# Performance work log

Measured on AMD Instinct MI355X. Metric: run time of the kernel, lower is better.

## Reference

```python
import jax, jax.numpy as jnp
import numpy as np


def setup_inputs() -> dict:
    key = jax.random.key(0)
    k1, k2 = jax.random.split(key)
    inputs = jax.random.normal(k1, (32, 4096, 64), dtype=jnp.float32)
    embed = jax.random.normal(k2, (64, 1024), dtype=jnp.float32)  # [embed_dim, n_embed]
    return {"inputs": inputs, "embed": embed}


def reference(inputs, embed):
    # Eval-mode forward of VectorQuantizer (self.training == False, no EMA update).
    embed_dim, n_embed = embed.shape
    flat = inputs.reshape(-1, embed_dim)  # [N, D]
    # distances[n, k] = ||flat_n||^2 - 2 flat_n . e_k + ||e_k||^2
    distances = (
        jnp.sum(flat * flat, axis=1, keepdims=True)
        - 2.0 * (flat @ embed)
        + jnp.sum(embed * embed, axis=0, keepdims=True)
    )  # [N, n_embed]
    # torch.argmax(-distances, 1) == argmin(distances, 1) (same first-occurrence tie-break)
    encoding_indices = jnp.argmin(distances, axis=1)  # [N] int
    idx = encoding_indices.reshape(inputs.shape[:-1])  # [B, T]
    # quantize: F.embedding(idx, embed.T) -> gather rows of embed.T
    quantized = jnp.take(embed.T, idx, axis=0)  # [B, T, D]
    codes = jnp.concatenate([inputs, quantized], axis=-1)  # [B, T, 2D]
    # straight-through estimator
    quantized_st = inputs + jax.lax.stop_gradient(quantized - inputs)
    return quantized_st, codes, idx
```

## Files before the change

### kernel.cpp

```cpp
#include <hip/hip_runtime.h>

#define D 64
#define KCODES 1024
#define PTS_PER_BLK 256
#define MTILES 16
#define NT 4
#define CODE_CHUNKS 4
#define PTILES 512
#define WL_CAP 4096

typedef short bf16x8 __attribute__((ext_vector_type(8)));
typedef float f32x4 __attribute__((ext_vector_type(4)));

static __device__ __forceinline__ short f2bf(float f) {
  unsigned u = __float_as_uint(f);
  u += 0x7FFF + ((u >> 16) & 1);
  return (short)(u >> 16);
}

static __device__ __forceinline__ void evalExact(const float* __restrict__ inputs,
                                                 const float* __restrict__ embedT,
                                                 const float* __restrict__ en2,
                                                 const float* s_fn2,
                                                 int p0blk, int pl, int c,
                                                 unsigned long long* s_best) {
  int p = p0blk + pl;
  const float* f = inputs + (size_t)p * D;
  const float* e = embedT + (size_t)c * D;
  float a0 = 0.f, a1 = 0.f, a2 = 0.f, a3 = 0.f;
#pragma unroll
  for (int d = 0; d < D; d += 4) {
    a0 = fmaf(f[d + 0], e[d + 0], a0);
    a1 = fmaf(f[d + 1], e[d + 1], a1);
    a2 = fmaf(f[d + 2], e[d + 2], a2);
    a3 = fmaf(f[d + 3], e[d + 3], a3);
  }
  float dot = (a0 + a1) + (a2 + a3);
  float dist = fmaf(-2.f, dot, s_fn2[pl]) + en2[c];
  unsigned long long key = ((unsigned long long)__float_as_uint(dist) << 32) | (unsigned)c;
  atomicMin(&s_best[pl], key);
}

__global__ void __launch_bounds__(256) vq_prep(const float* __restrict__ embed,
                                               const float* __restrict__ inputs,
                                               float* __restrict__ embedT,
                                               unsigned short* __restrict__ embedTb,
                                               float* __restrict__ en2,
                                               int* __restrict__ en2max_bits,
                                               float* __restrict__ fn2,
                                               unsigned long long* __restrict__ best) {
  const int bid = blockIdx.x;
  const int tid = threadIdx.x;
  if (bid < KCODES / 256) {
    int k = bid * 256 + tid;
    float row[D];
    float s = 0.f;
#pragma unroll
    for (int d = 0; d < D; ++d) {
      float e = embed[d * KCODES + k];
      row[d] = e;
      s = fmaf(e, e, s);
    }
    en2[k] = s;
    float4* o4 = reinterpret_cast<float4*>(embedT + (size_t)k * D);
#pragma unroll
    for (int j = 0; j < 16; ++j)
      o4[j] = make_float4(row[4 * j], row[4 * j + 1], row[4 * j + 2], row[4 * j + 3]);
    unsigned us[32];
#pragma unroll
    for (int j = 0; j < 32; ++j) {
      unsigned lo = (unsigned short)f2bf(row[2 * j]);
      unsigned hi = (unsigned short)f2bf(row[2 * j + 1]);
      us[j] = lo | (hi << 16);
    }
    uint4* ob = reinterpret_cast<uint4*>(embedTb + (size_t)k * D);
#pragma unroll
    for (int j = 0; j < 8; ++j)
      ob[j] = make_uint4(us[4 * j], us[4 * j + 1], us[4 * j + 2], us[4 * j + 3]);
    float m = s;
#pragma unroll
    for (int off = 32; off; off >>= 1) m = fmaxf(m, __shfl_down(m, off, 64));
    if ((tid & 63) == 0) atomicMax(en2max_bits, __float_as_int(m));
  } else {
    int p = (bid - KCODES / 256) * 256 + tid;
    const float4* i4 = reinterpret_cast<const float4*>(inputs + (size_t)p * D);
    float s = 0.f;
#pragma unroll
    for (int j = 0; j < 16; ++j) {
      float4 v = i4[j];
      s = fmaf(v.x, v.x, s); s = fmaf(v.y, v.y, s);
      s = fmaf(v.z, v.z, s); s = fmaf(v.w, v.w, s);
    }
    fn2[p] = s;
    best[p] = ~0ull;
  }
}

__global__ void __launch_bounds__(256, 4) vq_partial(
    const float* __restrict__ inputs, const float* __restrict__ embedT,
    const unsigned short* __restrict__ embedTb, const float* __restrict__ en2,
    const float* __restrict__ fn2, const int* __restrict__ en2max_bits,
    unsigned long long* __restrict__ best) {
  __shared__ unsigned long long s_best[PTS_PER_BLK];
  __shared__ unsigned s_wl[WL_CAP];
  __shared__ int s_wcount;
  __shared__ float s_fn2[PTS_PER_BLK];
  __shared__ float s_wmin[4][16];

  const int tid = threadIdx.x;
  const int w = tid >> 6;
  const int l = tid & 63;
  const int l15 = l & 15;
  const int lg = l >> 4;
  const int chunk = blockIdx.x / PTILES;
  const int ptile = blockIdx.x % PTILES;
  const int p0blk = ptile * PTS_PER_BLK;
  const int cb = chunk * 256 + w * 64;

  s_best[tid] = ~0ull;
  if (tid == 0) s_wcount = 0;
  s_fn2[tid] = fn2[p0blk + tid];

  const float en2max = __int_as_float(*en2max_bits);

  bf16x8 bfr[NT][2];
  float en2v[NT];
#pragma unroll
  for (int t = 0; t < NT; ++t) {
    const bf16x8* bp = reinterpret_cast<const bf16x8*>(
        embedTb + (size_t)(cb + 16 * t + l15) * D + lg * 8);
    bfr[t][0] = bp[0];
    bfr[t][1] = bp[4];
    en2v[t] = en2[cb + 16 * t + l15];
  }

  __syncthreads();

#pragma unroll 1
  for (int mt = 0; mt < MTILES; ++mt) {
    const int p0 = p0blk + mt * 16;
    const float* arow = inputs + (size_t)(p0 + l15) * D + lg * 8;
    float4 a0 = *reinterpret_cast<const float4*>(arow + 0);
    float4 a1 = *reinterpret_cast<const float4*>(arow + 4);
    float4 a2 = *reinterpret_cast<const float4*>(arow + 32);
    float4 a3 = *reinterpret_cast<const float4*>(arow + 36);
    bf16x8 af0, af1;
    af0[0] = f2bf(a0.x); af0[1] = f2bf(a0.y); af0[2] = f2bf(a0.z); af0[3] = f2bf(a0.w);
    af0[4] = f2bf(a1.x); af0[5] = f2bf(a1.y); af0[6] = f2bf(a1.z); af0[7] = f2bf(a1.w);
    af1[0] = f2bf(a2.x); af1[1] = f2bf(a2.y); af1[2] = f2bf(a2.z); af1[3] = f2bf(a2.w);
    af1[4] = f2bf(a3.x); af1[5] = f2bf(a3.y); af1[6] = f2bf(a3.z); af1[7] = f2bf(a3.w);

    f32x4 acc[NT];
#pragma unroll
    for (int t = 0; t < NT; ++t) acc[t] = (f32x4){0.f, 0.f, 0.f, 0.f};
#pragma unroll
    for (int t = 0; t < NT; ++t)
      acc[t] = __builtin_amdgcn_mfma_f32_16x16x32_bf16(af0, bfr[t][0], acc[t], 0, 0, 0);
#pragma unroll
    for (int t = 0; t < NT; ++t)
      acc[t] = __builtin_amdgcn_mfma_f32_16x16x32_bf16(af1, bfr[t][1], acc[t], 0, 0, 0);

    float fnv[4];
#pragma unroll
    for (int r = 0; r < 4; ++r) fnv[r] = s_fn2[mt * 16 + lg * 4 + r];
#pragma unroll
    for (int t = 0; t < NT; ++t)
#pragma unroll
      for (int r = 0; r < 4; ++r)
        acc[t][r] = fmaf(-2.f, acc[t][r], fnv[r]) + en2v[t];

    float m[4];
#pragma unroll
    for (int r = 0; r < 4; ++r) {
      float mm = acc[0][r];
#pragma unroll
      for (int t = 1; t < NT; ++t) mm = fminf(mm, acc[t][r]);
#pragma unroll
      for (int s = 1; s < 16; s <<= 1) mm = fminf(mm, __shfl_xor(mm, s, 16));
      m[r] = mm;
    }
    if (l15 == 0) {
#pragma unroll
      for (int r = 0; r < 4; ++r) s_wmin[w][lg * 4 + r] = m[r];
    }
    __syncthreads();
    float thr[4];
#pragma unroll
    for (int r = 0; r < 4; ++r) {
      int q = lg * 4 + r;
      float fm = fminf(fminf(s_wmin[0][q], s_wmin[1][q]), fminf(s_wmin[2][q], s_wmin[3][q]));
      thr[r] = fm + (0.03125f * sqrtf(fnv[r] * en2max) + 0.01f);
    }
#pragma unroll
    for (int t = 0; t < NT; ++t)
#pragma unroll
      for (int r = 0; r < 4; ++r)
        if (acc[t][r] <= thr[r]) {
          int pl = mt * 16 + lg * 4 + r;
          int c = cb + 16 * t + l15;
          int pos = atomicAdd(&s_wcount, 1);
          if (pos < WL_CAP) s_wl[pos] = (unsigned)((pl << 10) | c);
          else evalExact(inputs, embedT, en2, s_fn2, p0blk, pl, c, s_best);
        }
    __syncthreads();
  }

  int wc = s_wcount; if (wc > WL_CAP) wc = WL_CAP;
  for (int i = tid; i < wc; i += 256)
    evalExact(inputs, embedT, en2, s_fn2, p0blk, (int)(s_wl[i] >> 10), (int)(s_wl[i] & 1023), s_best);
  __syncthreads();

  atomicMin(&best[p0blk + tid], s_best[tid]);
}

__global__ void __launch_bounds__(256) vq_finalize(
    const float* __restrict__ inputs, const float* __restrict__ embedT,
    const unsigned long long* __restrict__ best,
    float* __restrict__ out_q, float* __restrict__ out_codes,
    float* __restrict__ out_idx) {
  const int tid = threadIdx.x;
  const int p0blk = blockIdx.x * 256;
  const int sub = tid & 3;
#pragma unroll 1
  for (int pass = 0; pass < 4; ++pass) {
    int pl = pass * 64 + (tid >> 2);
    int p = p0blk + pl;
    unsigned long long key = best[p];
    int c = (int)(unsigned)(key & 0xFFFFFFFFu);
    const f32x4* qrow = reinterpret_cast<const f32x4*>(embedT + (size_t)c * D);
    const f32x4* frow = reinterpret_cast<const f32x4*>(inputs + (size_t)p * D);
    f32x4* oq = reinterpret_cast<f32x4*>(out_q + (size_t)p * D);
    f32x4* oc = reinterpret_cast<f32x4*>(out_codes + (size_t)p * 2 * D);
#pragma unroll
    for (int j = 0; j < 4; ++j) {
      int i4 = j * 4 + sub;
      f32x4 qv = qrow[i4];
      f32x4 fv = frow[i4];
      oq[i4] = qv;
      oc[i4] = fv;
      oc[16 + i4] = qv;
    }
    if (sub == 0) out_idx[p] = (float)c;
  }
}

extern "C" void kernel_launch(void* const* d_in, const int* in_sizes, int n_in,
                              void* d_out, int out_size, void* d_ws, size_t ws_size,
                              hipStream_t stream) {
  const float* inputs = (const float*)d_in[0];
  const float* embed  = (const float*)d_in[1];
  int N = in_sizes[0] / D;

  unsigned long long* best = (unsigned long long*)d_ws;
  float* embedT            = (float*)(best + N);
  unsigned short* embedTb  = (unsigned short*)(embedT + KCODES * D);
  float* en2               = (float*)(embedTb + KCODES * D);
  float* fn2               = en2 + KCODES;
  int* en2max_bits         = (int*)(fn2 + N);

  float* out = (float*)d_out;
  float* out_q     = out;
  float* out_codes = out + (size_t)N * D;
  float* out_idx   = out + (size_t)N * D * 3;

  vq_prep<<<KCODES / 256 + N / 256, 256, 0, stream>>>(embed, inputs, embedT, embedTb,
                                                      en2, en2max_bits, fn2, best);
  vq_partial<<<CODE_CHUNKS * PTILES, 256, 0, stream>>>(inputs, embedT, embedTb, en2,
                                                       fn2, en2max_bits, best);
  vq_finalize<<<N / 256, 256, 0, stream>>>(inputs, embedT, best, out_q, out_codes, out_idx);
}
```

Measured before the change: 340.6 us.

## Switch VQ candidate filter to fp16 MFMA with tighter margin and double-buffered minima

Replaces the bf16 conversion and MFMA with fp16, whose extra mantissa bits allow an eightfold smaller error margin in the candidate threshold. This should leave far fewer candidates for exact fp32 re-evaluation. The per-point norm is dropped from the per-element distance because it is constant per row, and the per-tile minima buffer is double-buffered so the trailing barrier can be removed. The risks are fp16 overflow or range loss on large inputs, which could break the correctness bound, and the halved worklist capacity that pushes overflow candidates into inline exact evaluation.

Measured after the change: 314.4 us. 7.7% less time.

```diff
diff --git a/kernel.cpp b/kernel.cpp
--- a/kernel.cpp
+++ b/kernel.cpp
@@ -7,15 +7,14 @@
 #define NT 4
 #define CODE_CHUNKS 4
 #define PTILES 512
-#define WL_CAP 4096
-
-typedef short bf16x8 __attribute__((ext_vector_type(8)));
+#define WL_CAP 2048
+
+typedef _Float16 f16x8 __attribute__((ext_vector_type(8)));
 typedef float f32x4 __attribute__((ext_vector_type(4)));
 
-static __device__ __forceinline__ short f2bf(float f) {
-  unsigned u = __float_as_uint(f);
-  u += 0x7FFF + ((u >> 16) & 1);
-  return (short)(u >> 16);
+static __device__ __forceinline__ unsigned short f2h(float f) {
+  _Float16 h = (_Float16)f;
+  return __builtin_bit_cast(unsigned short, h);
 }
 
 static __device__ __forceinline__ void evalExact(const float* __restrict__ inputs,
@@ -44,7 +43,7 @@
 __global__ void __launch_bounds__(256) vq_prep(const float* __restrict__ embed,
                                                const float* __restrict__ inputs,
                                                float* __restrict__ embedT,
-                                               unsigned short* __restrict__ embedTb,
+                                               unsigned short* __restrict__ embedTh,
                                                float* __restrict__ en2,
                                                int* __restrict__ en2max_bits,
                                                float* __restrict__ fn2,
@@ -69,11 +68,11 @@
     unsigned us[32];
 #pragma unroll
     for (int j = 0; j < 32; ++j) {
-      unsigned lo = (unsigned short)f2bf(row[2 * j]);
-      unsigned hi = (unsigned short)f2bf(row[2 * j + 1]);
+      unsigned lo = f2h(row[2 * j]);
+      unsigned hi = f2h(row[2 * j + 1]);
       us[j] = lo | (hi << 16);
     }
-    uint4* ob = reinterpret_cast<uint4*>(embedTb + (size_t)k * D);
+    uint4* ob = reinterpret_cast<uint4*>(embedTh + (size_t)k * D);
 #pragma unroll
     for (int j = 0; j < 8; ++j)
       ob[j] = make_uint4(us[4 * j], us[4 * j + 1], us[4 * j + 2], us[4 * j + 3]);
@@ -98,14 +97,14 @@
 
 __global__ void __launch_bounds__(256, 4) vq_partial(
     const float* __restrict__ inputs, const float* __restrict__ embedT,
-    const unsigned short* __restrict__ embedTb, const float* __restrict__ en2,
+    const unsigned short* __restrict__ embedTh, const float* __restrict__ en2,
     const float* __restrict__ fn2, const int* __restrict__ en2max_bits,
     unsigned long long* __restrict__ best) {
   __shared__ unsigned long long s_best[PTS_PER_BLK];
   __shared__ unsigned s_wl[WL_CAP];
   __shared__ int s_wcount;
   __shared__ float s_fn2[PTS_PER_BLK];
-  __shared__ float s_wmin[4][16];
+  __shared__ float s_wmin[2][4][16];
 
   const int tid = threadIdx.x;
   const int w = tid >> 6;
@@ -123,12 +122,12 @@
 
   const float en2max = __int_as_float(*en2max_bits);
 
-  bf16x8 bfr[NT][2];
+  f16x8 bfr[NT][2];
   float en2v[NT];
 #pragma unroll
   for (int t = 0; t < NT; ++t) {
-    const bf16x8* bp = reinterpret_cast<const bf16x8*>(
-        embedTb + (size_t)(cb + 16 * t + l15) * D + lg * 8);
+    const f16x8* bp = reinterpret_cast<const f16x8*>(
+        embedTh + (size_t)(cb + 16 * t + l15) * D + lg * 8);
     bfr[t][0] = bp[0];
     bfr[t][1] = bp[4];
     en2v[t] = en2[cb + 16 * t + l15];
@@ -144,30 +143,27 @@
     float4 a1 = *reinterpret_cast<const float4*>(arow + 4);
     float4 a2 = *reinterpret_cast<const float4*>(arow + 32);
     float4 a3 = *reinterpret_cast<const float4*>(arow + 36);
-    bf16x8 af0, af1;
-    af0[0] = f2bf(a0.x); af0[1] = f2bf(a0.y); af0[2] = f2bf(a0.z); af0[3] = f2bf(a0.w);
-    af0[4] = f2bf(a1.x); af0[5] = f2bf(a1.y); af0[6] = f2bf(a1.z); af0[7] = f2bf(a1.w);
-    af1[0] = f2bf(a2.x); af1[1] = f2bf(a2.y); af1[2] = f2bf(a2.z); af1[3] = f2bf(a2.w);
-    af1[4] = f2bf(a3.x); af1[5] = f2bf(a3.y); af1[6] = f2bf(a3.z); af1[7] = f2bf(a3.w);
+    f16x8 af0, af1;
+    af0[0] = (_Float16)a0.x; af0[1] = (_Float16)a0.y; af0[2] = (_Float16)a0.z; af0[3] = (_Float16)a0.w;
+    af0[4] = (_Float16)a1.x; af0[5] = (_Float16)a1.y; af0[6] = (_Float16)a1.z; af0[7] = (_Float16)a1.w;
+    af1[0] = (_Float16)a2.x; af1[1] = (_Float16)a2.y; af1[2] = (_Float16)a2.z; af1[3] = (_Float16)a2.w;
+    af1[4] = (_Float16)a3.x; af1[5] = (_Float16)a3.y; af1[6] = (_Float16)a3.z; af1[7] = (_Float16)a3.w;
 
     f32x4 acc[NT];
 #pragma unroll
     for (int t = 0; t < NT; ++t) acc[t] = (f32x4){0.f, 0.f, 0.f, 0.f};
 #pragma unroll
     for (int t = 0; t < NT; ++t)
-      acc[t] = __builtin_amdgcn_mfma_f32_16x16x32_bf16(af0, bfr[t][0], acc[t], 0, 0, 0);
-#pragma unroll
-    for (int t = 0; t < NT; ++t)
-      acc[t] = __builtin_amdgcn_mfma_f32_16x16x32_bf16(af1, bfr[t][1], acc[t], 0, 0, 0);
-
-    float fnv[4];
-#pragma unroll
-    for (int r = 0; r < 4; ++r) fnv[r] = s_fn2[mt * 16 + lg * 4 + r];
+      acc[t] = __builtin_amdgcn_mfma_f32_16x16x32_f16(af0, bfr[t][0], acc[t], 0, 0, 0);
+#pragma unroll
+    for (int t = 0; t < NT; ++t)
+      acc[t] = __builtin_amdgcn_mfma_f32_16x16x32_f16(af1, bfr[t][1], acc[t], 0, 0, 0);
+
 #pragma unroll
     for (int t = 0; t < NT; ++t)
 #pragma unroll
       for (int r = 0; r < 4; ++r)
-        acc[t][r] = fmaf(-2.f, acc[t][r], fnv[r]) + en2v[t];
+        acc[t][r] = fmaf(-2.f, acc[t][r], en2v[t]);
 
     float m[4];
 #pragma unroll
@@ -181,15 +177,19 @@
     }
     if (l15 == 0) {
 #pragma unroll
-      for (int r = 0; r < 4; ++r) s_wmin[w][lg * 4 + r] = m[r];
+      for (int r = 0; r < 4; ++r) s_wmin[mt & 1][w][lg * 4 + r] = m[r];
     }
     __syncthreads();
+    float fnv[4];
+#pragma unroll
+    for (int r = 0; r < 4; ++r) fnv[r] = s_fn2[mt * 16 + lg * 4 + r];
     float thr[4];
 #pragma unroll
     for (int r = 0; r < 4; ++r) {
       int q = lg * 4 + r;
-      float fm = fminf(fminf(s_wmin[0][q], s_wmin[1][q]), fminf(s_wmin[2][q], s_wmin[3][q]));
-      thr[r] = fm + (0.03125f * sqrtf(fnv[r] * en2max) + 0.01f);
+      float fm = fminf(fminf(s_wmin[mt & 1][0][q], s_wmin[mt & 1][1][q]),
+                       fminf(s_wmin[mt & 1][2][q], s_wmin[mt & 1][3][q]));
+      thr[r] = fm + (0.00390625f * sqrtf(fnv[r] * en2max) + 0.01f);
     }
 #pragma unroll
     for (int t = 0; t < NT; ++t)
@@ -202,8 +202,9 @@
           if (pos < WL_CAP) s_wl[pos] = (unsigned)((pl << 10) | c);
           else evalExact(inputs, embedT, en2, s_fn2, p0blk, pl, c, s_best);
         }
-    __syncthreads();
-  }
+  }
+
+  __syncthreads();
 
   int wc = s_wcount; if (wc > WL_CAP) wc = WL_CAP;
   for (int i = tid; i < wc; i += 256)
@@ -251,21 +252,21 @@
   const float* embed  = (const float*)d_in[1];
   int N = in_sizes[0] / D;
 
-  unsigned long long* best = (unsigned long long*)d_ws;
-  float* embedT            = (float*)(best + N);
-  unsigned short* embedTb  = (unsigned short*)(embedT + KCODES * D);
-  float* en2               = (float*)(embedTb + KCODES * D);
-  float* fn2               = en2 + KCODES;
-  int* en2max_bits         = (int*)(fn2 + N);
+  unsigned long long* best  = (unsigned long long*)d_ws;
+  float* embedT             = (float*)(best + N);
+  unsigned short* embedTh   = (unsigned short*)(embedT + KCODES * D);
+  float* en2                = (float*)(embedTh + KCODES * D);
+  float* fn2                = en2 + KCODES;
+  int* en2max_bits          = (int*)(fn2 + N);
 
   float* out = (float*)d_out;
   float* out_q     = out;
   float* out_codes = out + (size_t)N * D;
   float* out_idx   = out + (size_t)N * D * 3;
 
-  vq_prep<<<KCODES / 256 + N / 256, 256, 0, stream>>>(embed, inputs, embedT, embedTb,
+  vq_prep<<<KCODES / 256 + N / 256, 256, 0, stream>>>(embed, inputs, embedT, embedTh,
                                                       en2, en2max_bits, fn2, best);
-  vq_partial<<<CODE_CHUNKS * PTILES, 256, 0, stream>>>(inputs, embedT, embedTb, en2,
+  vq_partial<<<CODE_CHUNKS * PTILES, 256, 0, stream>>>(inputs, embedT, embedTh, en2,
                                                        fn2, en2max_bits, best);
   vq_finalize<<<N / 256, 256, 0, stream>>>(inputs, embedT, best, out_q, out_codes, out_idx);
 }
```
